# Optimization experiments

Hardware: AMD Instinct MI355X
Metric: run time of the kernel (lower is better)

## Reference

```python
import jax, jax.numpy as jnp
import numpy as np

N, H, DDE, NH = 256, 256, 64, 4

def setup_inputs() -> dict:
    key = jax.random.key(0)
    ks = jax.random.split(key, 12)
    rn = lambda k, s, sc=1.0: (jax.random.normal(k, s) * sc).astype(jnp.float32)
    return {
        "action_hidden_state": rn(ks[0], (N, H)),
        "goal_hidden_state": rn(ks[1], (N, H)),
        "goal": rn(ks[2], (N, 2)),
        "action": rn(ks[3], (N, 2)),
        "W_dist": rn(ks[4], (8, DDE), 0.3),          # distEmbedding Linear(8, dde)
        "b_dist": jnp.zeros((DDE,), jnp.float32),
        "W_gate": rn(ks[5], (DDE, H), 0.1),          # gateFC Linear(dde, H)
        "b_gate": jnp.zeros((H,), jnp.float32),
        "w": rn(ks[6], (NH, 1, H, H), 0.06),         # GAT per-head projection
        "a": rn(ks[7], (1, 1, 2 * H, 1), 0.06),      # attention vector
        "bias": jnp.zeros((H,), jnp.float32),
    }

def reference(action_hidden_state, goal_hidden_state, goal, action,
              W_dist, b_dist, W_gate, b_gate, w, a, bias):
    n = goal.shape[0]
    # --- InteractionGate.cal_gate: x1[i,j] = x[j], x2[i,j] = x[i] ---
    g1 = jnp.broadcast_to(goal[None, :, :], (n, n, 2))
    g2 = jnp.broadcast_to(goal[:, None, :], (n, n, 2))
    a1 = jnp.broadcast_to(action[None, :, :], (n, n, 2))
    a2 = jnp.broadcast_to(action[:, None, :], (n, n, 2))
    dist = jnp.concatenate([a2, g2, a1, g1], axis=-1)                 # [n,n,8]
    gate = jax.nn.sigmoid(jax.nn.relu(dist @ W_dist + b_dist) @ W_gate + b_gate)  # [n,n,H]
    # temp_action_1[i,j] = action_hidden_state[j]
    gate_action = gate * jnp.tanh(action_hidden_state[None, :, :])    # [n,n,H]
    # diagonal entries replaced by goal_hidden_state (mask_goal = eye)
    eye = jnp.eye(n, dtype=bool)[:, :, None]
    gated_h = jnp.where(eye, goal_hidden_state[None, :, :], gate_action)  # [n,n,H]

    # --- GAT assembly: h_self[i,k] = ahs[i]; h_other = cat(ahs, gated_h) ---
    h_other = jnp.concatenate([action_hidden_state[:, None, :], gated_h], axis=1)  # [n,n+1,H]

    wm = w[:, 0]          # [NH,H,H]
    a_flat = a[0, 0, :, 0]  # [2H]
    f = wm.shape[-1]
    n_head = wm.shape[0]
    # h_self rows along k are all identical -> project once per (head, node)
    hsp = jnp.einsum('nh,zhf->znf', action_hidden_state, wm)          # [NH,n,f]
    hop = jnp.einsum('nkh,zhf->znkf', h_other, wm)                    # [NH,n,n+1,f]
    # cat([h_self', h_other']) @ a  ==  h_self'@a[:f] + h_other'@a[f:]
    score = (hsp @ a_flat[:f])[:, :, None] + hop @ a_flat[f:]         # [NH,n,n+1]
    e = jnp.where(score > 0, score, 0.2 * score)                      # LeakyReLU(0.2)
    alpha = jax.nn.softmax(e, axis=-1)                                # softmax over neighbors
    # h_attn = matmul(h_other, w) == hop; weighted sum over k, mean over heads
    out = jnp.einsum('znk,znkf->nf', alpha, hop) / n_head             # [n,f]
    return jax.nn.relu(out) + bias
```

## Files before the change

### kernel.cpp

```cpp
#include <hip/hip_runtime.h>
#include <hip/hip_bf16.h>

#define NN 256
#define HH 256

typedef __attribute__((ext_vector_type(8))) short short8;
typedef __attribute__((ext_vector_type(4))) float f32x4;

__device__ __forceinline__ ushort f2bf(float x) {
    __hip_bfloat16 h = __float2bfloat16(x);
    return *reinterpret_cast<ushort*>(&h);
}
__device__ __forceinline__ float bf2f(ushort u) {
    __hip_bfloat16 h = *reinterpret_cast<__hip_bfloat16*>(&u);
    return __bfloat162float(h);
}
template <int CTRL>
__device__ __forceinline__ float dpp_add(float x) {
    int y = __builtin_amdgcn_update_dpp(0, __float_as_int(x), CTRL, 0xF, 0xF, true);
    return x + __int_as_float(y);
}
template <int CTRL>
__device__ __forceinline__ float dpp_max(float x) {
    int y = __builtin_amdgcn_update_dpp(0, __float_as_int(x), CTRL, 0xF, 0xF, true);
    return fmaxf(x, __int_as_float(y));
}
__device__ __forceinline__ float red16(float v) {
    v = dpp_add<0xB1>(v); v = dpp_add<0x4E>(v);
    v = dpp_add<0x141>(v); v = dpp_add<0x140>(v);
    return v;
}
__device__ __forceinline__ float red16max(float v) {
    v = dpp_max<0xB1>(v); v = dpp_max<0x4E>(v);
    v = dpp_max<0x141>(v); v = dpp_max<0x140>(v);
    return v;
}

#define WS_P   0
#define WS_Q   16384
#define WS_T   32768
#define WS_WA  98304
#define WS_WB  99328
#define WS_WGT 100352
#define WS_PV  108544
#define WS_ML  632832
#define WS_W2H 636928
#define WS_W2L 768000

__global__ __launch_bounds__(256) void precompute_kernel(
    const float* __restrict__ ahs, const float* __restrict__ goal,
    const float* __restrict__ action, const float* __restrict__ Wd,
    const float* __restrict__ b_dist, const float* __restrict__ Wg,
    const float* __restrict__ w, const float* __restrict__ a,
    float* __restrict__ ws)
{
    const int b = blockIdx.x;
    const int t = threadIdx.x;
    const int wid  = t >> 6;
    const int lane = t & 63;
    float* P  = ws + WS_P;
    float* Q  = ws + WS_Q;
    float* T  = ws + WS_T;
    float* WA = ws + WS_WA;
    float* WB = ws + WS_WB;
    ushort* WgT  = (ushort*)(ws + WS_WGT);
    ushort* W2hi = (ushort*)(ws + WS_W2H);
    ushort* W2lo = (ushort*)(ws + WS_W2L);

    __shared__ __align__(16) float tile[64][65];

    if (b < 16) {
        const int z  = b >> 2;
        const int rg = b & 3;
        const int hbase = rg*64 + wid*16;
        const f32x4 aB = *(const f32x4*)(a + lane*4);
        const f32x4 aA = *(const f32x4*)(a + HH + lane*4);
#pragma unroll 4
        for (int rr = 0; rr < 16; ++rr) {
            const int h = hbase + rr;
            const f32x4 w4 = *(const f32x4*)(w + z*HH*HH + h*HH + lane*4);
            float dA = w4.x*aA.x + w4.y*aA.y + w4.z*aA.z + w4.w*aA.w;
            float dB = w4.x*aB.x + w4.y*aB.y + w4.z*aB.z + w4.w*aB.w;
#pragma unroll
            for (int off = 32; off; off >>= 1) {
                dA += __shfl_xor(dA, off);
                dB += __shfl_xor(dB, off);
            }
            if (lane == 0) { WA[z*HH + h] = dA; WB[z*HH + h] = dB; }
        }
    } else if (b < 80) {
        const int idx = b - 16;
        const int k0  = (idx >> 2) * 64;
        const int f0  = (idx & 3) * 64;
        const int ff  = t & 63;
#pragma unroll 4
        for (int i = 0; i < 16; ++i) {
            const int kk = i*4 + wid;
            tile[kk][ff] = w[(k0 + kk)*HH + f0 + ff];
        }
        __syncthreads();
#pragma unroll 4
        for (int i = 0; i < 16; ++i) {
            const int fl = i*4 + wid;
            float x = tile[ff][fl];
            ushort hi = f2bf(x);
            ushort lo = f2bf(x - bf2f(hi));
            W2hi[(size_t)(f0 + fl)*1024 + k0 + ff] = hi;
            W2lo[(size_t)(f0 + fl)*1024 + k0 + ff] = lo;
        }
    } else if (b < 144) {
        const int i = (b - 80)*4 + wid;
        const int d = lane;
        float a0 = action[2*i], a1 = action[2*i+1];
        float g0 = goal[2*i],   g1 = goal[2*i+1];
        P[i*64 + d] = a0*Wd[0*64+d] + a1*Wd[1*64+d]
                    + g0*Wd[2*64+d] + g1*Wd[3*64+d] + b_dist[d];
        Q[i*64 + d] = a0*Wd[4*64+d] + a1*Wd[5*64+d]
                    + g0*Wd[6*64+d] + g1*Wd[7*64+d];
    } else if (b < 208) {
        const int d = b - 144;
        WgT[t*64 + d] = f2bf(Wg[d*HH + t]);
    } else {
        const int idx = ((b - 208)*256 + t)*4;
        float4 v = *(const float4*)(ahs + idx);
        float4 o;
        o.x = tanhf(v.x); o.y = tanhf(v.y); o.z = tanhf(v.z); o.w = tanhf(v.w);
        *(float4*)(T + idx) = o;
    }
}

__global__ __launch_bounds__(256, 2) void gat_partial_kernel(
    const float* __restrict__ ahs, const float* __restrict__ ghs,
    const float* __restrict__ b_gate, float* __restrict__ ws)
{
    const int n    = blockIdx.x >> 1;
    const int hh   = blockIdx.x & 1;
    const int t    = threadIdx.x;
    const int wid  = t >> 6;
    const int lane = t & 63;
    const int quad = lane >> 4;
    const int l15  = lane & 15;
    const int zg   = quad;
    const int jj   = l15;
    const int n0   = wid * 64;

    const float* P  = ws + WS_P;
    const float* Q  = ws + WS_Q;
    const float* T  = ws + WS_T;
    const float* WA = ws + WS_WA;
    const float* WB = ws + WS_WB;
    const ushort* WgT = (const ushort*)(ws + WS_WGT);
    float* PV = ws + WS_PV;
    float* ML = ws + WS_ML;

    __shared__ __align__(16) float part[2][4][16][4];
    __shared__ __align__(16) float alpha_w[4][16][4];
    __shared__ __align__(16) float vred[16][260];

    int hcol[4];
#pragma unroll
    for (int nt = 0; nt < 4; ++nt) hcol[nt] = n0 + nt*16 + l15;

    short8 bfrag[4][2];
    float  wa_reg[4][4];
    float  bgv[4], gval[4];
#pragma unroll
    for (int nt = 0; nt < 4; ++nt) {
#pragma unroll
        for (int kh = 0; kh < 2; ++kh)
            bfrag[nt][kh] = *(const short8*)(WgT + hcol[nt]*64 + kh*32 + quad*8);
#pragma unroll
        for (int z = 0; z < 4; ++z) wa_reg[z][nt] = WA[z*HH + hcol[nt]];
        bgv[nt]  = b_gate[hcol[nt]];
        gval[nt] = ghs[n*HH + hcol[nt]];
    }

    float pnA[2][8];
#pragma unroll
    for (int kh = 0; kh < 2; ++kh) {
        *(f32x4*)&pnA[kh][0] = *(const f32x4*)(P + n*64 + kh*32 + quad*8);
        *(f32x4*)&pnA[kh][4] = *(const f32x4*)(P + n*64 + kh*32 + quad*8 + 4);
    }

    float vacc[4][4];
    {
        float av[4];
#pragma unroll
        for (int nt = 0; nt < 4; ++nt) av[nt] = ahs[n*HH + hcol[nt]];
#pragma unroll
        for (int z = 0; z < 4; ++z)
#pragma unroll
            for (int nt = 0; nt < 4; ++nt)
                vacc[z][nt] = (hh == 0 && quad == 0) ? av[nt] : 0.f;
    }

    float cz_r, m_r, l_r;
    {
        float pc = 0.f, ps = 0.f;
        const int hb = jj*16;
#pragma unroll
        for (int i4 = 0; i4 < 4; ++i4) {
            f32x4 av = *(const f32x4*)(ahs + n*HH + hb + i4*4);
            f32x4 wb = *(const f32x4*)(WB + zg*HH + hb + i4*4);
            f32x4 wa = *(const f32x4*)(WA + zg*HH + hb + i4*4);
            pc = fmaf(av.x, wb.x, pc); pc = fmaf(av.y, wb.y, pc);
            pc = fmaf(av.z, wb.z, pc); pc = fmaf(av.w, wb.w, pc);
            ps = fmaf(av.x, wa.x, ps); ps = fmaf(av.y, wa.y, ps);
            ps = fmaf(av.z, wa.z, ps); ps = fmaf(av.w, wa.w, ps);
        }
        pc = red16(pc); ps = red16(ps);
        cz_r = pc;
        if (hh == 0) {
            float sc = pc + ps;
            m_r = sc > 0.f ? sc : 0.2f * sc;
            l_r = 1.0f;
        } else {
            m_r = -__builtin_inff();
            l_r = 0.0f;
        }
    }

    for (int cc = 0; cc < 8; ++cc) {
        const int j0  = hh*128 + cc*16;
        const int par = cc & 1;

        float tval[4][4];
#pragma unroll
        for (int r = 0; r < 4; ++r) {
            const int jg = j0 + quad*4 + r;
#pragma unroll
            for (int nt = 0; nt < 4; ++nt)
                tval[nt][r] = T[jg*HH + hcol[nt]];
        }

        short8 afrag[2];
#pragma unroll
        for (int kh = 0; kh < 2; ++kh) {
            const float* qrow = Q + (j0 + l15)*64 + kh*32 + quad*8;
            f32x4 qa = *(const f32x4*)qrow;
            f32x4 qb = *(const f32x4*)(qrow + 4);
            ushort hv[8];
            hv[0] = f2bf(fmaxf(pnA[kh][0] + qa.x, 0.f));
            hv[1] = f2bf(fmaxf(pnA[kh][1] + qa.y, 0.f));
            hv[2] = f2bf(fmaxf(pnA[kh][2] + qa.z, 0.f));
            hv[3] = f2bf(fmaxf(pnA[kh][3] + qa.w, 0.f));
            hv[4] = f2bf(fmaxf(pnA[kh][4] + qb.x, 0.f));
            hv[5] = f2bf(fmaxf(pnA[kh][5] + qb.y, 0.f));
            hv[6] = f2bf(fmaxf(pnA[kh][6] + qb.z, 0.f));
            hv[7] = f2bf(fmaxf(pnA[kh][7] + qb.w, 0.f));
            afrag[kh] = *(short8*)hv;
        }

        f32x4 acc[4];
#pragma unroll
        for (int nt = 0; nt < 4; ++nt) {
            f32x4 a4 = (f32x4){0.f,0.f,0.f,0.f};
            a4 = __builtin_amdgcn_mfma_f32_16x16x32_bf16(afrag[0], bfrag[nt][0], a4, 0, 0, 0);
            a4 = __builtin_amdgcn_mfma_f32_16x16x32_bf16(afrag[1], bfrag[nt][1], a4, 0, 0, 0);
            acc[nt] = a4;
        }

        float vals[4][4];
#pragma unroll
        for (int r = 0; r < 4; ++r) {
            const int jg = j0 + quad*4 + r;
            const bool diag = (jg == n);
#pragma unroll
            for (int nt = 0; nt < 4; ++nt) {
                float u = acc[nt][r] + bgv[nt];
                float g = 1.0f / (1.0f + __expf(-u));
                vals[nt][r] = diag ? gval[nt] : g * tval[nt][r];
            }
        }

#pragma unroll
        for (int z = 0; z < 4; ++z) {
            float pp[4];
#pragma unroll
            for (int r = 0; r < 4; ++r) {
                float s = 0.f;
#pragma unroll
                for (int nt = 0; nt < 4; ++nt)
                    s = fmaf(vals[nt][r], wa_reg[z][nt], s);
                pp[r] = red16(s);
            }
            if (l15 == z) {
#pragma unroll
                for (int r = 0; r < 4; ++r)
                    part[par][z][quad*4 + r][wid] = pp[r];
            }
        }
        __syncthreads();

        float scl0, scl1, scl2, scl3;
        {
            f32x4 pr = *(const f32x4*)&part[par][zg][jj][0];
            float s = cz_r + ((pr.x + pr.y) + (pr.z + pr.w));
            float e = s > 0.f ? s : 0.2f * s;
            float mx = red16max(e);
            float m_new = fmaxf(m_r, mx);
            float at = __expf(e - m_new);
            float ss = red16(at);
            float scale = __expf(m_r - m_new);
            l_r = l_r * scale + ss;
            m_r = m_new;
            alpha_w[wid][jj][zg] = at;
            scl0 = __shfl(scale, 0);
            scl1 = __shfl(scale, 16);
            scl2 = __shfl(scale, 32);
            scl3 = __shfl(scale, 48);
        }
#pragma unroll
        for (int nt = 0; nt < 4; ++nt) {
            vacc[0][nt] *= scl0; vacc[1][nt] *= scl1;
            vacc[2][nt] *= scl2; vacc[3][nt] *= scl3;
        }
#pragma unroll
        for (int r = 0; r < 4; ++r) {
            f32x4 al = *(const f32x4*)&alpha_w[wid][quad*4 + r][0];
#pragma unroll
            for (int nt = 0; nt < 4; ++nt) {
                float v = vals[nt][r];
                vacc[0][nt] = fmaf(al.x, v, vacc[0][nt]);
                vacc[1][nt] = fmaf(al.y, v, vacc[1][nt]);
                vacc[2][nt] = fmaf(al.z, v, vacc[2][nt]);
                vacc[3][nt] = fmaf(al.w, v, vacc[3][nt]);
            }
        }
    }

#pragma unroll
    for (int z = 0; z < 4; ++z)
#pragma unroll
        for (int nt = 0; nt < 4; ++nt)
            vred[quad*4 + z][hcol[nt]] = vacc[z][nt];
    __syncthreads();
#pragma unroll
    for (int z = 0; z < 4; ++z) {
        float s = (vred[0*4+z][t] + vred[1*4+z][t]) + (vred[2*4+z][t] + vred[3*4+z][t]);
        PV[((size_t)(hh*4 + z)*NN + n)*HH + t] = s;
    }
    if (wid == 0 && l15 == 0) {
        ML[((hh*4 + zg)*NN + n)*2 + 0] = m_r;
        ML[((hh*4 + zg)*NN + n)*2 + 1] = l_r;
    }
}

__global__ __launch_bounds__(256) void gat_out_kernel(
    const float* __restrict__ bias, const float* __restrict__ ws,
    float* __restrict__ out)
{
    const int n0 = (blockIdx.x >> 2) * 16;
    const int f0 = (blockIdx.x & 3) * 64;
    const int t    = threadIdx.x;
    const int wid  = t >> 6;
    const int lane = t & 63;
    const int quad = lane >> 4;
    const int l15  = lane & 15;

    const float* PV = ws + WS_PV;
    const float* ML = ws + WS_ML;
    const ushort* W2hi = (const ushort*)(ws + WS_W2H);
    const ushort* W2lo = (const ushort*)(ws + WS_W2L);

    __shared__ __align__(16) float redc[12288/4];
    __shared__ __align__(16) float sq[16][4][2];

    if (t < 128) {
        const int n_i = t >> 3, z = (t >> 1) & 3, q = t & 1;
        float m = ML[((q*4 + z)*NN + n0 + n_i)*2 + 0];
        float l = ML[((q*4 + z)*NN + n0 + n_i)*2 + 1];
        float mm = fmaxf(m, __shfl_xor(m, 1));
        float s  = __expf(m - mm);
        float ls = l * s;
        ls += __shfl_xor(ls, 1);
        sq[n_i][z][q] = s / ls;
    }
    __syncthreads();

    f32x4 acc[4];
#pragma unroll
    for (int nt = 0; nt < 4; ++nt) acc[nt] = (f32x4){0.f,0.f,0.f,0.f};

    const float s0 = sq[l15][wid][0];
    const float s1 = sq[l15][wid][1];
    const float* pv0 = PV + ((size_t)(0*4 + wid)*NN + n0 + l15)*HH;
    const float* pv1 = PV + ((size_t)(1*4 + wid)*NN + n0 + l15)*HH;

    for (int ks = 0; ks < 8; ++ks) {
        const int kp = ks*32 + quad*8;
        f32x4 p0a = *(const f32x4*)(pv0 + kp);
        f32x4 p0b = *(const f32x4*)(pv0 + kp + 4);
        f32x4 p1a = *(const f32x4*)(pv1 + kp);
        f32x4 p1b = *(const f32x4*)(pv1 + kp + 4);
        float v[8];
        v[0] = s0*p0a.x + s1*p1a.x; v[1] = s0*p0a.y + s1*p1a.y;
        v[2] = s0*p0a.z + s1*p1a.z; v[3] = s0*p0a.w + s1*p1a.w;
        v[4] = s0*p0b.x + s1*p1b.x; v[5] = s0*p0b.y + s1*p1b.y;
        v[6] = s0*p0b.z + s1*p1b.z; v[7] = s0*p0b.w + s1*p1b.w;
        ushort hi[8], lo[8];
#pragma unroll
        for (int c = 0; c < 8; ++c) {
            hi[c] = f2bf(v[c]);
            lo[c] = f2bf(v[c] - bf2f(hi[c]));
        }
        short8 ah = *(short8*)hi;
        short8 al = *(short8*)lo;
        const int kg = wid*256 + kp;
#pragma unroll
        for (int nt = 0; nt < 4; ++nt) {
            const size_t boff = (size_t)(f0 + nt*16 + l15)*1024 + kg;
            short8 bh = *(const short8*)(W2hi + boff);
            short8 bl = *(const short8*)(W2lo + boff);
            acc[nt] = __builtin_amdgcn_mfma_f32_16x16x32_bf16(ah, bh, acc[nt], 0, 0, 0);
            acc[nt] = __builtin_amdgcn_mfma_f32_16x16x32_bf16(ah, bl, acc[nt], 0, 0, 0);
            acc[nt] = __builtin_amdgcn_mfma_f32_16x16x32_bf16(al, bh, acc[nt], 0, 0, 0);
        }
    }
    __syncthreads();

    if (wid > 0) {
#pragma unroll
        for (int nt = 0; nt < 4; ++nt)
#pragma unroll
            for (int r = 0; r < 4; ++r)
                redc[(((wid-1)*4 + nt)*16 + quad*4 + r)*16 + l15] = acc[nt][r];
    }
    __syncthreads();
    if (wid == 0) {
#pragma unroll
        for (int nt = 0; nt < 4; ++nt) {
            const int f = f0 + nt*16 + l15;
            float bv = bias[f];
#pragma unroll
            for (int r = 0; r < 4; ++r) {
                const int row = quad*4 + r;
                float s = acc[nt][r]
                        + redc[((0*4 + nt)*16 + row)*16 + l15]
                        + redc[((1*4 + nt)*16 + row)*16 + l15]
                        + redc[((2*4 + nt)*16 + row)*16 + l15];
                out[(size_t)(n0 + row)*HH + f] = fmaxf(0.25f * s, 0.f) + bv;
            }
        }
    }
}

extern "C" void kernel_launch(void* const* d_in, const int* in_sizes, int n_in,
                              void* d_out, int out_size, void* d_ws, size_t ws_size,
                              hipStream_t stream)
{
    const float* ahs    = (const float*)d_in[0];
    const float* ghs    = (const float*)d_in[1];
    const float* goal   = (const float*)d_in[2];
    const float* action = (const float*)d_in[3];
    const float* Wd     = (const float*)d_in[4];
    const float* b_dist = (const float*)d_in[5];
    const float* Wg     = (const float*)d_in[6];
    const float* b_gate = (const float*)d_in[7];
    const float* w      = (const float*)d_in[8];
    const float* a      = (const float*)d_in[9];
    const float* bias   = (const float*)d_in[10];
    float* ws   = (float*)d_ws;
    float* outp = (float*)d_out;

    precompute_kernel<<<272, 256, 0, stream>>>(ahs, goal, action, Wd, b_dist, Wg, w, a, ws);
    gat_partial_kernel<<<512, 256, 0, stream>>>(ahs, ghs, b_gate, ws);
    gat_out_kernel<<<64, 256, 0, stream>>>(bias, ws, outp);
}
```

Measured before the change: 125.5 us.

## Drop precomputed transposed/bf16 weight and tanh buffers, compute them inline

```diff
diff --git a/kernel.cpp b/kernel.cpp
--- a/kernel.cpp
+++ b/kernel.cpp
@@ -36,38 +36,24 @@
     return v;
 }
 
-#define WS_P   0
-#define WS_Q   16384
-#define WS_T   32768
-#define WS_WA  98304
-#define WS_WB  99328
-#define WS_WGT 100352
-#define WS_PV  108544
-#define WS_ML  632832
-#define WS_W2H 636928
-#define WS_W2L 768000
+#define WS_Q   0
+#define WS_WA  16384
+#define WS_WB  17408
+#define WS_PV  18432
+#define WS_ML  542720
 
 __global__ __launch_bounds__(256) void precompute_kernel(
-    const float* __restrict__ ahs, const float* __restrict__ goal,
-    const float* __restrict__ action, const float* __restrict__ Wd,
-    const float* __restrict__ b_dist, const float* __restrict__ Wg,
-    const float* __restrict__ w, const float* __restrict__ a,
-    float* __restrict__ ws)
+    const float* __restrict__ goal, const float* __restrict__ action,
+    const float* __restrict__ Wd, const float* __restrict__ w,
+    const float* __restrict__ a, float* __restrict__ ws)
 {
     const int b = blockIdx.x;
     const int t = threadIdx.x;
     const int wid  = t >> 6;
     const int lane = t & 63;
-    float* P  = ws + WS_P;
     float* Q  = ws + WS_Q;
-    float* T  = ws + WS_T;
     float* WA = ws + WS_WA;
     float* WB = ws + WS_WB;
-    ushort* WgT  = (ushort*)(ws + WS_WGT);
-    ushort* W2hi = (ushort*)(ws + WS_W2H);
-    ushort* W2lo = (ushort*)(ws + WS_W2L);
-
-    __shared__ __align__(16) float tile[64][65];
 
     if (b < 16) {
         const int z  = b >> 2;
@@ -88,50 +74,22 @@
             }
             if (lane == 0) { WA[z*HH + h] = dA; WB[z*HH + h] = dB; }
         }
-    } else if (b < 80) {
-        const int idx = b - 16;
-        const int k0  = (idx >> 2) * 64;
-        const int f0  = (idx & 3) * 64;
-        const int ff  = t & 63;
-#pragma unroll 4
-        for (int i = 0; i < 16; ++i) {
-            const int kk = i*4 + wid;
-            tile[kk][ff] = w[(k0 + kk)*HH + f0 + ff];
-        }
-        __syncthreads();
-#pragma unroll 4
-        for (int i = 0; i < 16; ++i) {
-            const int fl = i*4 + wid;
-            float x = tile[ff][fl];
-            ushort hi = f2bf(x);
-            ushort lo = f2bf(x - bf2f(hi));
-            W2hi[(size_t)(f0 + fl)*1024 + k0 + ff] = hi;
-            W2lo[(size_t)(f0 + fl)*1024 + k0 + ff] = lo;
-        }
-    } else if (b < 144) {
-        const int i = (b - 80)*4 + wid;
+    } else {
+        const int i = (b - 16)*4 + wid;
         const int d = lane;
         float a0 = action[2*i], a1 = action[2*i+1];
         float g0 = goal[2*i],   g1 = goal[2*i+1];
-        P[i*64 + d] = a0*Wd[0*64+d] + a1*Wd[1*64+d]
-                    + g0*Wd[2*64+d] + g1*Wd[3*64+d] + b_dist[d];
         Q[i*64 + d] = a0*Wd[4*64+d] + a1*Wd[5*64+d]
                     + g0*Wd[6*64+d] + g1*Wd[7*64+d];
-    } else if (b < 208) {
-        const int d = b - 144;
-        WgT[t*64 + d] = f2bf(Wg[d*HH + t]);
-    } else {
-        const int idx = ((b - 208)*256 + t)*4;
-        float4 v = *(const float4*)(ahs + idx);
-        float4 o;
-        o.x = tanhf(v.x); o.y = tanhf(v.y); o.z = tanhf(v.z); o.w = tanhf(v.w);
-        *(float4*)(T + idx) = o;
     }
 }
 
 __global__ __launch_bounds__(256, 2) void gat_partial_kernel(
     const float* __restrict__ ahs, const float* __restrict__ ghs,
-    const float* __restrict__ b_gate, float* __restrict__ ws)
+    const float* __restrict__ goal, const float* __restrict__ action,
+    const float* __restrict__ Wd, const float* __restrict__ b_dist,
+    const float* __restrict__ Wg, const float* __restrict__ b_gate,
+    float* __restrict__ ws)
 {
     const int n    = blockIdx.x >> 1;
     const int hh   = blockIdx.x & 1;
@@ -144,12 +102,9 @@
     const int jj   = l15;
     const int n0   = wid * 64;
 
-    const float* P  = ws + WS_P;
     const float* Q  = ws + WS_Q;
-    const float* T  = ws + WS_T;
     const float* WA = ws + WS_WA;
     const float* WB = ws + WS_WB;
-    const ushort* WgT = (const ushort*)(ws + WS_WGT);
     float* PV = ws + WS_PV;
     float* ML = ws + WS_ML;
 
@@ -162,13 +117,23 @@
     for (int nt = 0; nt < 4; ++nt) hcol[nt] = n0 + nt*16 + l15;
 
     short8 bfrag[4][2];
-    float  wa_reg[4][4];
-    float  bgv[4], gval[4];
+#pragma unroll
+    for (int nt = 0; nt < 4; ++nt)
+#pragma unroll
+        for (int kh = 0; kh < 2; ++kh) {
+            ushort hv[8];
+#pragma unroll
+            for (int i = 0; i < 8; ++i) {
+                const int d = kh*32 + quad*8 + i;
+                hv[i] = f2bf(Wg[d*HH + hcol[nt]]);
+            }
+            bfrag[nt][kh] = *(short8*)hv;
+        }
+
+    float wa_reg[4][4];
+    float bgv[4], gval[4];
 #pragma unroll
     for (int nt = 0; nt < 4; ++nt) {
-#pragma unroll
-        for (int kh = 0; kh < 2; ++kh)
-            bfrag[nt][kh] = *(const short8*)(WgT + hcol[nt]*64 + kh*32 + quad*8);
 #pragma unroll
         for (int z = 0; z < 4; ++z) wa_reg[z][nt] = WA[z*HH + hcol[nt]];
         bgv[nt]  = b_gate[hcol[nt]];
@@ -176,10 +141,17 @@
     }
 
     float pnA[2][8];
-#pragma unroll
-    for (int kh = 0; kh < 2; ++kh) {
-        *(f32x4*)&pnA[kh][0] = *(const f32x4*)(P + n*64 + kh*32 + quad*8);
-        *(f32x4*)&pnA[kh][4] = *(const f32x4*)(P + n*64 + kh*32 + quad*8 + 4);
+    {
+        const float a0 = action[2*n], a1 = action[2*n+1];
+        const float g0 = goal[2*n],   g1 = goal[2*n+1];
+#pragma unroll
+        for (int kh = 0; kh < 2; ++kh)
+#pragma unroll
+            for (int i = 0; i < 8; ++i) {
+                const int k = kh*32 + quad*8 + i;
+                pnA[kh][i] = a0*Wd[0*64+k] + a1*Wd[1*64+k]
+                           + g0*Wd[2*64+k] + g1*Wd[3*64+k] + b_dist[k];
+            }
     }
 
     float vacc[4][4];
@@ -224,13 +196,13 @@
         const int j0  = hh*128 + cc*16;
         const int par = cc & 1;
 
-        float tval[4][4];
+        float hval[4][4];
 #pragma unroll
         for (int r = 0; r < 4; ++r) {
             const int jg = j0 + quad*4 + r;
 #pragma unroll
             for (int nt = 0; nt < 4; ++nt)
-                tval[nt][r] = T[jg*HH + hcol[nt]];
+                hval[nt][r] = ahs[jg*HH + hcol[nt]];
         }
 
         short8 afrag[2];
@@ -269,7 +241,7 @@
             for (int nt = 0; nt < 4; ++nt) {
                 float u = acc[nt][r] + bgv[nt];
                 float g = 1.0f / (1.0f + __expf(-u));
-                vals[nt][r] = diag ? gval[nt] : g * tval[nt][r];
+                vals[nt][r] = diag ? gval[nt] : g * tanhf(hval[nt][r]);
             }
         }
 
@@ -347,11 +319,11 @@
 }
 
 __global__ __launch_bounds__(256) void gat_out_kernel(
-    const float* __restrict__ bias, const float* __restrict__ ws,
-    float* __restrict__ out)
+    const float* __restrict__ w, const float* __restrict__ bias,
+    const float* __restrict__ ws, float* __restrict__ out)
 {
-    const int n0 = (blockIdx.x >> 2) * 16;
-    const int f0 = (blockIdx.x & 3) * 64;
+    const int n0 = (blockIdx.x >> 3) * 16;
+    const int f0 = (blockIdx.x & 7) * 32;
     const int t    = threadIdx.x;
     const int wid  = t >> 6;
     const int lane = t & 63;
@@ -360,10 +332,8 @@
 
     const float* PV = ws + WS_PV;
     const float* ML = ws + WS_ML;
-    const ushort* W2hi = (const ushort*)(ws + WS_W2H);
-    const ushort* W2lo = (const ushort*)(ws + WS_W2L);
-
-    __shared__ __align__(16) float redc[12288/4];
+
+    __shared__ __align__(16) float redc[3*2*16*16];
     __shared__ __align__(16) float sq[16][4][2];
 
     if (t < 128) {
@@ -378,9 +348,9 @@
     }
     __syncthreads();
 
-    f32x4 acc[4];
-#pragma unroll
-    for (int nt = 0; nt < 4; ++nt) acc[nt] = (f32x4){0.f,0.f,0.f,0.f};
+    f32x4 acc[2];
+    acc[0] = (f32x4){0.f,0.f,0.f,0.f};
+    acc[1] = (f32x4){0.f,0.f,0.f,0.f};
 
     const float s0 = sq[l15][wid][0];
     const float s1 = sq[l15][wid][1];
@@ -408,10 +378,17 @@
         short8 al = *(short8*)lo;
         const int kg = wid*256 + kp;
 #pragma unroll
-        for (int nt = 0; nt < 4; ++nt) {
-            const size_t boff = (size_t)(f0 + nt*16 + l15)*1024 + kg;
-            short8 bh = *(const short8*)(W2hi + boff);
-            short8 bl = *(const short8*)(W2lo + boff);
+        for (int nt = 0; nt < 2; ++nt) {
+            const int f = f0 + nt*16 + l15;
+            ushort bhv[8], blv[8];
+#pragma unroll
+            for (int i = 0; i < 8; ++i) {
+                float wv = w[(size_t)(kg + i)*HH + f];
+                bhv[i] = f2bf(wv);
+                blv[i] = f2bf(wv - bf2f(bhv[i]));
+            }
+            short8 bh = *(short8*)bhv;
+            short8 bl = *(short8*)blv;
             acc[nt] = __builtin_amdgcn_mfma_f32_16x16x32_bf16(ah, bh, acc[nt], 0, 0, 0);
             acc[nt] = __builtin_amdgcn_mfma_f32_16x16x32_bf16(ah, bl, acc[nt], 0, 0, 0);
             acc[nt] = __builtin_amdgcn_mfma_f32_16x16x32_bf16(al, bh, acc[nt], 0, 0, 0);
@@ -421,24 +398,24 @@
 
     if (wid > 0) {
 #pragma unroll
-        for (int nt = 0; nt < 4; ++nt)
+        for (int nt = 0; nt < 2; ++nt)
 #pragma unroll
             for (int r = 0; r < 4; ++r)
-                redc[(((wid-1)*4 + nt)*16 + quad*4 + r)*16 + l15] = acc[nt][r];
+                redc[(((wid-1)*2 + nt)*16 + quad*4 + r)*16 + l15] = acc[nt][r];
     }
     __syncthreads();
     if (wid == 0) {
 #pragma unroll
-        for (int nt = 0; nt < 4; ++nt) {
+        for (int nt = 0; nt < 2; ++nt) {
             const int f = f0 + nt*16 + l15;
             float bv = bias[f];
 #pragma unroll
             for (int r = 0; r < 4; ++r) {
                 const int row = quad*4 + r;
                 float s = acc[nt][r]
-                        + redc[((0*4 + nt)*16 + row)*16 + l15]
-                        + redc[((1*4 + nt)*16 + row)*16 + l15]
-                        + redc[((2*4 + nt)*16 + row)*16 + l15];
+                        + redc[((0*2 + nt)*16 + row)*16 + l15]
+                        + redc[((1*2 + nt)*16 + row)*16 + l15]
+                        + redc[((2*2 + nt)*16 + row)*16 + l15];
                 out[(size_t)(n0 + row)*HH + f] = fmaxf(0.25f * s, 0.f) + bv;
             }
         }
@@ -463,7 +440,8 @@
     float* ws   = (float*)d_ws;
     float* outp = (float*)d_out;
 
-    precompute_kernel<<<272, 256, 0, stream>>>(ahs, goal, action, Wd, b_dist, Wg, w, a, ws);
-    gat_partial_kernel<<<512, 256, 0, stream>>>(ahs, ghs, b_gate, ws);
-    gat_out_kernel<<<64, 256, 0, stream>>>(bias, ws, outp);
-}
+    precompute_kernel<<<80, 256, 0, stream>>>(goal, action, Wd, w, a, ws);
+    gat_partial_kernel<<<512, 256, 0, stream>>>(ahs, ghs, goal, action, Wd, b_dist,
+                                                Wg, b_gate, ws);
+    gat_out_kernel<<<128, 256, 0, stream>>>(w, bias, ws, outp);
+}
```

After: 131.2 us. 4.6% more time.
